# Kernel tuning notes

Hardware: AMD Instinct MI355X
Metric: run time of the kernel (lower is better)

## Reference

```python
import jax, jax.numpy as jnp
import numpy as np

B, T, D, H, V = 256, 32, 500, 1024, 8000
NF = 512  # conv output channels per window size


def setup_inputs() -> dict:
    key = jax.random.key(0)
    ks = jax.random.split(key, 20)
    s = 0.02
    inp = {
        "text": jax.random.normal(ks[0], (B, T, D), jnp.float32),
        "text_bow": jax.random.uniform(ks[1], (B, V), jnp.float32),
        "text_lengths": jax.random.randint(ks[2], (B,), 1, T + 1).astype(jnp.int32),
        # GRU forward direction (PyTorch layout: [3H, D], [3H, H], gates r,z,n)
        "Wih_f": jax.random.normal(ks[3], (3 * H, D), jnp.float32) * s,
        "Whh_f": jax.random.normal(ks[4], (3 * H, H), jnp.float32) * s,
        "bih_f": jax.random.normal(ks[5], (3 * H,), jnp.float32) * s,
        "bhh_f": jax.random.normal(ks[6], (3 * H,), jnp.float32) * s,
        # GRU backward direction
        "Wih_b": jax.random.normal(ks[7], (3 * H, D), jnp.float32) * s,
        "Whh_b": jax.random.normal(ks[8], (3 * H, H), jnp.float32) * s,
        "bih_b": jax.random.normal(ks[9], (3 * H,), jnp.float32) * s,
        "bhh_b": jax.random.normal(ks[10], (3 * H,), jnp.float32) * s,
        # reduce linear: 2H -> H
        "W_red": jax.random.normal(ks[11], (H, 2 * H), jnp.float32) * s,
        "b_red": jax.random.normal(ks[12], (H,), jnp.float32) * s,
        # conv kernels, reshaped from Conv2d [512,1,ws,2H] to 1D conv [512, 2H, ws]
        "conv_w2": jax.random.normal(ks[13], (NF, 2 * H, 2), jnp.float32) * s,
        "conv_b2": jax.random.normal(ks[14], (NF,), jnp.float32) * s,
        "conv_w3": jax.random.normal(ks[15], (NF, 2 * H, 3), jnp.float32) * s,
        "conv_b3": jax.random.normal(ks[16], (NF,), jnp.float32) * s,
        "conv_w4": jax.random.normal(ks[17], (NF, 2 * H, 4), jnp.float32) * s,
        "conv_b4": jax.random.normal(ks[18], (NF,), jnp.float32) * s,
    }
    return inp


def _run_gru_dir(x, lengths, Wih, Whh, bih, bhh, reverse):
    """One GRU direction over padded [B,T,D] with packed-sequence semantics:
    outputs are zero at t >= length (as pad_packed_sequence produces)."""
    b, t, _ = x.shape
    h_dim = Whh.shape[1]
    xg = jnp.einsum('btd,gd->btg', x, Wih) + bih  # [B,T,3H] input projections
    valid = jnp.arange(t)[None, :] < lengths[:, None]  # [B,T]

    def step(h, inp):
        xg_t, v = inp  # [B,3H], [B]
        hg = h @ Whh.T + bhh
        xr, xz, xn = jnp.split(xg_t, 3, axis=-1)
        hr, hz, hn = jnp.split(hg, 3, axis=-1)
        r = jax.nn.sigmoid(xr + hr)
        z = jax.nn.sigmoid(xz + hz)
        n = jnp.tanh(xn + r * hn)
        h_new = (1.0 - z) * n + z * h
        h_new = jnp.where(v[:, None], h_new, h)
        out = jnp.where(v[:, None], h_new, 0.0)
        return h_new, out

    h0 = jnp.zeros((b, h_dim), x.dtype)
    xs = (jnp.swapaxes(xg, 0, 1), valid.T)  # time-major
    _, outs = jax.lax.scan(step, h0, xs, reverse=reverse)
    return jnp.swapaxes(outs, 0, 1)  # [B,T,H]


def _conv_branch(x_c, w, b, ws):
    # x_c: [B, 2H, T]; w: [512, 2H, ws]; 'same-padding-both-sides' (ws-1) like Conv2d padding=(ws-1,0)
    y = jax.lax.conv_general_dilated(
        x_c, w, window_strides=(1,), padding=[(ws - 1, ws - 1)],
        dimension_numbers=('NCH', 'OIH', 'NCH')) + b[None, :, None]
    y = jax.nn.leaky_relu(y, 0.01)
    return jnp.max(y, axis=-1)  # global max-pool over time -> [B,512]


def reference(text, text_bow, text_lengths, Wih_f, Whh_f, bih_f, bhh_f,
              Wih_b, Whh_b, bih_b, bhh_b, W_red, b_red,
              conv_w2, conv_b2, conv_w3, conv_b3, conv_w4, conv_b4):
    out_f = _run_gru_dir(text, text_lengths, Wih_f, Whh_f, bih_f, bhh_f, reverse=False)
    out_b = _run_gru_dir(text, text_lengths, Wih_b, Whh_b, bih_b, bhh_b, reverse=True)
    gru_init_out = jnp.concatenate([out_f, out_b], axis=-1)  # [B,T,2H]

    # masked mean pooling over valid timesteps (the per-sample Python loop)
    mask = (jnp.arange(gru_init_out.shape[1])[None, :] < text_lengths[:, None]).astype(gru_init_out.dtype)
    gru_mean = jnp.sum(gru_init_out * mask[:, :, None], axis=1) / text_lengths[:, None].astype(gru_init_out.dtype)
    gru_out = gru_mean @ W_red.T + b_red  # [B,H] (dropout is identity at eval)

    x_c = jnp.swapaxes(gru_init_out, 1, 2)  # [B,2H,T]
    con_out = jnp.concatenate([
        _conv_branch(x_c, conv_w2, conv_b2, 2),
        _conv_branch(x_c, conv_w3, conv_b3, 3),
        _conv_branch(x_c, conv_w4, conv_b4, 4),
    ], axis=1)  # [B,1536]

    return jnp.concatenate([gru_out, con_out, text_bow], axis=1)  # [B, H+1536+V]
```

## Files before the change

### kernel.cpp

```cpp
#include <hip/hip_runtime.h>
#include <hip/hip_bf16.h>
#include <math.h>

#define B_ 256
#define T_ 32
#define D_ 500
#define H_ 1024
#define V_ 8000
#define NF_ 512
#define G3H (3*H_)
#define H2 (2*H_)
#define OUTC (H_ + 3*NF_ + V_)
#define KPAD 512
#define NTAP 9
#define NCAT (NTAP*NF_)
#define MS 512
#define WFRAG_G (64*32*512)

typedef float f32x4 __attribute__((ext_vector_type(4)));
typedef short bf16x8 __attribute__((ext_vector_type(8)));

static __device__ __forceinline__ short f2b(float f) {
    unsigned u = __float_as_uint(f);
    unsigned r = (u + 0x7fffu + ((u >> 16) & 1u)) >> 16;
    return (short)r;
}
static __device__ __forceinline__ float b2f(short s) {
    return __uint_as_float(((unsigned)(unsigned short)s) << 16);
}

__global__ __launch_bounds__(256) void gemm_bt(
    const short* __restrict__ A, int lda,
    const short* __restrict__ Bt, int ldb,
    const float* __restrict__ bias,
    void* __restrict__ Cv, int ldc,
    int K, int mode)
{
    __shared__ short As[128 * 32];
    __shared__ short Bs[128 * 32];
    const int tid  = threadIdx.x;
    const int w    = tid >> 6, lane = tid & 63;

    const int nbx = gridDim.x;
    const int nwg = nbx * gridDim.y;
    int flat = blockIdx.y * nbx + blockIdx.x;
    flat = (flat & 7) * (nwg >> 3) + (flat >> 3);
    const int m0 = (flat / nbx) * 128, n0 = (flat % nbx) * 128;

    const int wm   = (w >> 1) * 64, wn = (w & 1) * 64;

    f32x4 acc[4][4];
#pragma unroll
    for (int i = 0; i < 4; ++i)
#pragma unroll
        for (int j = 0; j < 4; ++j) acc[i][j] = (f32x4){0.f, 0.f, 0.f, 0.f};

    const int srow = w * 16 + (lane >> 2);
    const int scol = (lane & 3) * 8;
    const long aoff0 = (long)(m0 + srow) * lda + scol;
    const long aoff1 = (long)(m0 + srow + 64) * lda + scol;
    const long boff0 = (long)(n0 + srow) * ldb + scol;
    const long boff1 = (long)(n0 + srow + 64) * ldb + scol;
    short* lA0 = As + w * 512;        short* lA1 = As + 2048 + w * 512;
    short* lB0 = Bs + w * 512;        short* lB1 = Bs + 2048 + w * 512;

    const int fr = lane & 15, fk = (lane >> 4) * 8;

    for (int kt = 0; kt < K; kt += 32) {
        __builtin_amdgcn_global_load_lds((const __attribute__((address_space(1))) void*)(A + aoff0 + kt),
                                         (__attribute__((address_space(3))) void*)lA0, 16, 0, 0);
        __builtin_amdgcn_global_load_lds((const __attribute__((address_space(1))) void*)(A + aoff1 + kt),
                                         (__attribute__((address_space(3))) void*)lA1, 16, 0, 0);
        __builtin_amdgcn_global_load_lds((const __attribute__((address_space(1))) void*)(Bt + boff0 + kt),
                                         (__attribute__((address_space(3))) void*)lB0, 16, 0, 0);
        __builtin_amdgcn_global_load_lds((const __attribute__((address_space(1))) void*)(Bt + boff1 + kt),
                                         (__attribute__((address_space(3))) void*)lB1, 16, 0, 0);
        __syncthreads();
        bf16x8 af[4], bfv[4];
#pragma unroll
        for (int i = 0; i < 4; ++i) af[i]  = *(const bf16x8*)(As + (wm + i * 16 + fr) * 32 + fk);
#pragma unroll
        for (int j = 0; j < 4; ++j) bfv[j] = *(const bf16x8*)(Bs + (wn + j * 16 + fr) * 32 + fk);
#pragma unroll
        for (int i = 0; i < 4; ++i)
#pragma unroll
            for (int j = 0; j < 4; ++j)
                acc[i][j] = __builtin_amdgcn_mfma_f32_16x16x32_bf16(af[i], bfv[j], acc[i][j], 0, 0, 0);
        __syncthreads();
    }

    const int er = (lane >> 4) * 4;
    const int ec = lane & 15;
#pragma unroll
    for (int i = 0; i < 4; ++i) {
#pragma unroll
        for (int j = 0; j < 4; ++j) {
#pragma unroll
            for (int q = 0; q < 4; ++q) {
                const int m = m0 + wm + i * 16 + er + q;
                const int n = n0 + wn + j * 16 + ec;
                float v = acc[i][j][q];
                if (mode == 0) {
                    ((float*)Cv)[(long)m * ldc + n] = v + bias[n];
                } else if (mode == 2) {
                    ((short*)Cv)[(long)m * ldc + n] = f2b(v + bias[n]);
                } else {
                    ((_Float16*)Cv)[(long)m * ldc + n] = (_Float16)v;
                }
            }
        }
    }
}

__global__ void repack_whh(const float* __restrict__ src, short* __restrict__ dst)
{
    const int idx = blockIdx.x * 256 + threadIdx.x;
    const int l = idx & 63;
    const int kt = (idx >> 6) & 31;
    const int j16 = (idx >> 11) & 63;
    const int g = idx >> 17;
    const long srow = ((long)(g << 10) + (j16 << 4) + (l & 15)) * H_ + kt * 32 + ((l >> 4) << 3);
    short o[8];
#pragma unroll
    for (int e = 0; e < 8; ++e) o[e] = f2b(src[srow + e]);
    *(bf16x8*)&dst[(long)idx * 8] = *(bf16x8*)o;
}

__global__ __launch_bounds__(256) void gru_step_frag(
    const short* __restrict__ hbf_prev, short* __restrict__ hbf_next,
    const float* __restrict__ h32_prev, float* __restrict__ h32_next,
    const short* __restrict__ wfragf, const short* __restrict__ wfragb,
    const float* __restrict__ bhhf, const float* __restrict__ bhhb,
    const short* __restrict__ xgf, const short* __restrict__ xgb,
    short* __restrict__ gout, const int* __restrict__ lengths, int s)
{
    const int tid = threadIdx.x;
    const int w = tid >> 6, lane = tid & 63;
    const int bid = blockIdx.x;
    const int jt = bid & 31;
    const int mtd = bid >> 5;
    const int dir = mtd >> 2, mt = mtd & 3;
    const int m0 = dir * 256 + mt * 64;
    const int j0 = jt * 32;
    const int wm = (w >> 1) * 32, wj = (w & 1) * 16;
    const int tt = dir ? (T_ - 1 - s) : s;

    const short* wfrag = dir ? wfragb : wfragf;
    const float* bhh = dir ? bhhb : bhhf;
    const short* xg  = dir ? xgb : xgf;

    const int fr15 = lane & 15, fk8 = (lane >> 4) * 8;
    const long arow0 = (long)(m0 + wm + fr15) * H_ + fk8;
    const long arow1 = arow0 + (long)16 * H_;
    const int j16 = (j0 + wj) >> 4;
    const short* bbase = wfrag + ((long)j16 * 32) * 512 + lane * 8;

    f32x4 acc[3][2];
#pragma unroll
    for (int g = 0; g < 3; ++g)
#pragma unroll
        for (int i = 0; i < 2; ++i) acc[g][i] = (f32x4){0.f, 0.f, 0.f, 0.f};

#pragma unroll 4
    for (int kt = 0; kt < 32; ++kt) {
        const bf16x8 af0 = *(const bf16x8*)(hbf_prev + arow0 + kt * 32);
        const bf16x8 af1 = *(const bf16x8*)(hbf_prev + arow1 + kt * 32);
        const bf16x8 b0 = *(const bf16x8*)(bbase + (long)kt * 512);
        const bf16x8 b1 = *(const bf16x8*)(bbase + (long)kt * 512 + WFRAG_G);
        const bf16x8 b2 = *(const bf16x8*)(bbase + (long)kt * 512 + 2 * WFRAG_G);
        acc[0][0] = __builtin_amdgcn_mfma_f32_16x16x32_bf16(af0, b0, acc[0][0], 0, 0, 0);
        acc[0][1] = __builtin_amdgcn_mfma_f32_16x16x32_bf16(af1, b0, acc[0][1], 0, 0, 0);
        acc[1][0] = __builtin_amdgcn_mfma_f32_16x16x32_bf16(af0, b1, acc[1][0], 0, 0, 0);
        acc[1][1] = __builtin_amdgcn_mfma_f32_16x16x32_bf16(af1, b1, acc[1][1], 0, 0, 0);
        acc[2][0] = __builtin_amdgcn_mfma_f32_16x16x32_bf16(af0, b2, acc[2][0], 0, 0, 0);
        acc[2][1] = __builtin_amdgcn_mfma_f32_16x16x32_bf16(af1, b2, acc[2][1], 0, 0, 0);
    }

    const int er = (lane >> 4) * 4, ec = lane & 15;
    const int jj = j0 + wj + ec;
    const float bhr = bhh[jj], bhz = bhh[H_ + jj], bhn = bhh[2 * H_ + jj];

#pragma unroll
    for (int i = 0; i < 2; ++i) {
#pragma unroll
        for (int q = 0; q < 4; ++q) {
            const int m = m0 + wm + i * 16 + er + q;
            const int b = m & 255;
            const short* xrow = xg + ((long)b * T_ + tt) * G3H;
            const float xr = b2f(xrow[jj]);
            const float xz = b2f(xrow[H_ + jj]);
            const float xn = b2f(xrow[2 * H_ + jj]);
            const float rr = 1.f / (1.f + expf(-(xr + acc[0][i][q] + bhr)));
            const float zz = 1.f / (1.f + expf(-(xz + acc[1][i][q] + bhz)));
            const float nn = tanhf(xn + rr * (acc[2][i][q] + bhn));
            const long hidx = (long)m * H_ + jj;
            const float hp = h32_prev[hidx];
            const float hnew = (1.f - zz) * nn + zz * hp;
            const bool valid = tt < lengths[b];
            const float ho = valid ? hnew : hp;
            h32_next[hidx] = ho;
            hbf_next[hidx] = f2b(ho);
            gout[((long)b * T_ + tt) * H2 + (long)dir * H_ + jj] = valid ? f2b(hnew) : (short)0;
        }
    }
}

__global__ void f2b_pad(const float* __restrict__ src, short* __restrict__ dst,
                        int Ksrc, int Kdst)
{
    const int idx = blockIdx.x * 256 + threadIdx.x;
    const int r = idx / Kdst, c = idx % Kdst;
    dst[idx] = (c < Ksrc) ? f2b(src[(long)r * Ksrc + c]) : (short)0;
}

__global__ void repack_tap(const float* __restrict__ src, short* __restrict__ dst, int ws)
{
    const int idx = blockIdx.x * 256 + threadIdx.x;
    const int rem = idx % (NF_ * H2);
    const int k = idx / (NF_ * H2);
    const int f = rem >> 11, c = rem & 2047;
    dst[idx] = f2b(src[((long)(f << 11) + c) * ws + k]);
}

__global__ void mean_pool2(const short* __restrict__ gin,
                           const int* __restrict__ lengths,
                           short* __restrict__ mean_bf)
{
    const int idx = blockIdx.x * 256 + threadIdx.x;
    const int b = idx >> 11, c = idx & 2047;
    float s = 0.f;
#pragma unroll
    for (int t = 0; t < T_; ++t) s += b2f(gin[((long)(b * T_ + t)) * H2 + c]);
    mean_bf[idx] = f2b(s / (float)lengths[b]);
}

__global__ void conv_max(const _Float16* __restrict__ P,
                         const float* __restrict__ cb2, const float* __restrict__ cb3,
                         const float* __restrict__ cb4, float* __restrict__ out)
{
    const int idx = blockIdx.x * 256 + threadIdx.x;
    const int b = idx / 1536, u0 = idx % 1536;
    int Tout, ws, base, f; float bias;
    if (u0 < 512)       { ws = 2; Tout = 33; base = 0;    f = u0;        bias = cb2[f]; }
    else if (u0 < 1024) { ws = 3; Tout = 34; base = 1024; f = u0 - 512;  bias = cb3[f]; }
    else                { ws = 4; Tout = 35; base = 2560; f = u0 - 1024; bias = cb4[f]; }
    const _Float16* Pb = P + (long)b * T_ * NCAT + base + f;
    float m = -INFINITY;
    for (int u = 0; u < Tout; ++u) {
        float s = bias;
        for (int k = 0; k < ws; ++k) {
            const int t = u - (ws - 1) + k;
            if (t >= 0 && t < T_) s += (float)Pb[(long)t * NCAT + k * NF_];
        }
        s = s > 0.f ? s : 0.01f * s;
        m = fmaxf(m, s);
    }
    out[(long)b * OUTC + H_ + u0] = m;
}

__global__ void bow_copy(const float* __restrict__ bow, float* __restrict__ out)
{
    const int idx = blockIdx.x * 256 + threadIdx.x;
    const int b = idx / 2000, q = idx % 2000;
    const float4* src = (const float4*)(bow + (long)b * V_);
    float4* dst = (float4*)(out + (long)b * OUTC + H_ + 3 * NF_);
    dst[q] = src[q];
}

extern "C" void kernel_launch(void* const* d_in, const int* in_sizes, int n_in,
                              void* d_out, int out_size, void* d_ws, size_t ws_size,
                              hipStream_t stream)
{
    const float* text    = (const float*)d_in[0];
    const float* bow     = (const float*)d_in[1];
    const int*   lengths = (const int*)  d_in[2];
    const float* Wih_f   = (const float*)d_in[3];
    const float* Whh_f   = (const float*)d_in[4];
    const float* bih_f   = (const float*)d_in[5];
    const float* bhh_f   = (const float*)d_in[6];
    const float* Wih_b   = (const float*)d_in[7];
    const float* Whh_b   = (const float*)d_in[8];
    const float* bih_b   = (const float*)d_in[9];
    const float* bhh_b   = (const float*)d_in[10];
    const float* W_red   = (const float*)d_in[11];
    const float* b_red   = (const float*)d_in[12];
    const float* cw2     = (const float*)d_in[13];
    const float* cb2     = (const float*)d_in[14];
    const float* cw3     = (const float*)d_in[15];
    const float* cb3     = (const float*)d_in[16];
    const float* cw4     = (const float*)d_in[17];
    const float* cb4     = (const float*)d_in[18];
    float* out = (float*)d_out;

    char* ws = (char*)d_ws;
    size_t off = 0;
    short* xg_f = (short*)(ws + off); off += (size_t)B_ * T_ * G3H * 2;
    short* xg_b = (short*)(ws + off); off += (size_t)B_ * T_ * G3H * 2;
    _Float16* P    = (_Float16*)(char*)xg_f;
    short* wtap_bf = (short*)((char*)xg_f + (size_t)B_ * T_ * NCAT * 2);
    short* gin_bf = (short*)(ws + off); off += (size_t)B_ * T_ * H2 * 2;
    short* text_bf = gin_bf;
    short* wihf_bf = (short*)((char*)gin_bf + (size_t)B_ * T_ * KPAD * 2);
    short* wihb_bf = wihf_bf + (size_t)G3H * KPAD;
    short* wfragf  = (short*)(ws + off); off += (size_t)3 * WFRAG_G * 2;
    short* wfragb  = (short*)(ws + off); off += (size_t)3 * WFRAG_G * 2;
    short* wred_bf = (short*)(ws + off); off += (size_t)H_ * H2 * 2;
    float* h32     = (float*)(ws + off); off += (size_t)2 * MS * H_ * 4;
    short* h_bf    = (short*)(ws + off); off += (size_t)2 * MS * H_ * 2;
    short* gmean_bf= (short*)(ws + off); off += (size_t)B_ * H2 * 2;

    const dim3 blk(256);

    f2b_pad<<<dim3((B_ * T_ * KPAD) / 256), blk, 0, stream>>>(text, text_bf, D_, KPAD);
    f2b_pad<<<dim3((G3H * KPAD) / 256), blk, 0, stream>>>(Wih_f, wihf_bf, D_, KPAD);
    f2b_pad<<<dim3((G3H * KPAD) / 256), blk, 0, stream>>>(Wih_b, wihb_bf, D_, KPAD);
    f2b_pad<<<dim3((H_ * H2) / 256), blk, 0, stream>>>(W_red, wred_bf, H2, H2);
    repack_whh<<<dim3(1536), blk, 0, stream>>>(Whh_f, wfragf);
    repack_whh<<<dim3(1536), blk, 0, stream>>>(Whh_b, wfragb);

    gemm_bt<<<dim3(G3H / 128, (B_ * T_) / 128), blk, 0, stream>>>(
        text_bf, KPAD, wihf_bf, KPAD, bih_f, xg_f, G3H, KPAD, 2);
    gemm_bt<<<dim3(G3H / 128, (B_ * T_) / 128), blk, 0, stream>>>(
        text_bf, KPAD, wihb_bf, KPAD, bih_b, xg_b, G3H, KPAD, 2);

    hipMemsetAsync(h32, 0, (size_t)MS * H_ * 4, stream);
    hipMemsetAsync(h_bf, 0, (size_t)MS * H_ * 2, stream);
    for (int s = 0; s < T_; ++s) {
        const int cur = s & 1, nxt = (s + 1) & 1;
        gru_step_frag<<<dim3(256), blk, 0, stream>>>(
            h_bf + (size_t)cur * MS * H_, h_bf + (size_t)nxt * MS * H_,
            h32 + (size_t)cur * MS * H_, h32 + (size_t)nxt * MS * H_,
            wfragf, wfragb, bhh_f, bhh_b, xg_f, xg_b,
            gin_bf, lengths, s);
    }

    mean_pool2<<<dim3((B_ * H2) / 256), blk, 0, stream>>>(gin_bf, lengths, gmean_bf);
    gemm_bt<<<dim3(H_ / 128, B_ / 128), blk, 0, stream>>>(
        gmean_bf, H2, wred_bf, H2, b_red, out, OUTC, H2, 0);

    repack_tap<<<dim3((2 * NF_ * H2) / 256), blk, 0, stream>>>(cw2, wtap_bf, 2);
    repack_tap<<<dim3((3 * NF_ * H2) / 256), blk, 0, stream>>>(cw3, wtap_bf + (size_t)2 * NF_ * H2, 3);
    repack_tap<<<dim3((4 * NF_ * H2) / 256), blk, 0, stream>>>(cw4, wtap_bf + (size_t)5 * NF_ * H2, 4);
    gemm_bt<<<dim3(NCAT / 128, (B_ * T_) / 128), blk, 0, stream>>>(
        gin_bf, H2, wtap_bf, H2, nullptr, P, NCAT, H2, 3);

    conv_max<<<dim3((B_ * 1536) / 256), blk, 0, stream>>>(P, cb2, cb3, cb4, out);
    bow_copy<<<dim3((B_ * 2000) / 256), blk, 0, stream>>>(bow, out);
}
```

Before: 1.076 ms.

## Merge fwd/bwd input GEMMs and halve GRU step M-tile for more blocks

```diff
diff --git a/kernel.cpp b/kernel.cpp
--- a/kernel.cpp
+++ b/kernel.cpp
@@ -9,6 +9,7 @@
 #define V_ 8000
 #define NF_ 512
 #define G3H (3*H_)
+#define G6H (6*H_)
 #define H2 (2*H_)
 #define OUTC (H_ + 3*NF_ + V_)
 #define KPAD 512
@@ -131,49 +132,41 @@
     const float* __restrict__ h32_prev, float* __restrict__ h32_next,
     const short* __restrict__ wfragf, const short* __restrict__ wfragb,
     const float* __restrict__ bhhf, const float* __restrict__ bhhb,
-    const short* __restrict__ xgf, const short* __restrict__ xgb,
+    const short* __restrict__ xgcat,
     short* __restrict__ gout, const int* __restrict__ lengths, int s)
 {
     const int tid = threadIdx.x;
     const int w = tid >> 6, lane = tid & 63;
     const int bid = blockIdx.x;
     const int jt = bid & 31;
-    const int mtd = bid >> 5;
-    const int dir = mtd >> 2, mt = mtd & 3;
-    const int m0 = dir * 256 + mt * 64;
+    const int mq = bid >> 5;
+    const int dir = mq >> 3, mt = mq & 7;
+    const int m0 = dir * 256 + mt * 32;
     const int j0 = jt * 32;
-    const int wm = (w >> 1) * 32, wj = (w & 1) * 16;
+    const int wm = (w >> 1) * 16, wj = (w & 1) * 16;
     const int tt = dir ? (T_ - 1 - s) : s;
 
     const short* wfrag = dir ? wfragb : wfragf;
     const float* bhh = dir ? bhhb : bhhf;
-    const short* xg  = dir ? xgb : xgf;
 
     const int fr15 = lane & 15, fk8 = (lane >> 4) * 8;
-    const long arow0 = (long)(m0 + wm + fr15) * H_ + fk8;
-    const long arow1 = arow0 + (long)16 * H_;
+    const long arow = (long)(m0 + wm + fr15) * H_ + fk8;
     const int j16 = (j0 + wj) >> 4;
     const short* bbase = wfrag + ((long)j16 * 32) * 512 + lane * 8;
 
-    f32x4 acc[3][2];
-#pragma unroll
-    for (int g = 0; g < 3; ++g)
-#pragma unroll
-        for (int i = 0; i < 2; ++i) acc[g][i] = (f32x4){0.f, 0.f, 0.f, 0.f};
-
-#pragma unroll 4
+    f32x4 acc[3];
+#pragma unroll
+    for (int g = 0; g < 3; ++g) acc[g] = (f32x4){0.f, 0.f, 0.f, 0.f};
+
+#pragma unroll 8
     for (int kt = 0; kt < 32; ++kt) {
-        const bf16x8 af0 = *(const bf16x8*)(hbf_prev + arow0 + kt * 32);
-        const bf16x8 af1 = *(const bf16x8*)(hbf_prev + arow1 + kt * 32);
+        const bf16x8 af0 = *(const bf16x8*)(hbf_prev + arow + kt * 32);
         const bf16x8 b0 = *(const bf16x8*)(bbase + (long)kt * 512);
         const bf16x8 b1 = *(const bf16x8*)(bbase + (long)kt * 512 + WFRAG_G);
         const bf16x8 b2 = *(const bf16x8*)(bbase + (long)kt * 512 + 2 * WFRAG_G);
-        acc[0][0] = __builtin_amdgcn_mfma_f32_16x16x32_bf16(af0, b0, acc[0][0], 0, 0, 0);
-        acc[0][1] = __builtin_amdgcn_mfma_f32_16x16x32_bf16(af1, b0, acc[0][1], 0, 0, 0);
-        acc[1][0] = __builtin_amdgcn_mfma_f32_16x16x32_bf16(af0, b1, acc[1][0], 0, 0, 0);
-        acc[1][1] = __builtin_amdgcn_mfma_f32_16x16x32_bf16(af1, b1, acc[1][1], 0, 0, 0);
-        acc[2][0] = __builtin_amdgcn_mfma_f32_16x16x32_bf16(af0, b2, acc[2][0], 0, 0, 0);
-        acc[2][1] = __builtin_amdgcn_mfma_f32_16x16x32_bf16(af1, b2, acc[2][1], 0, 0, 0);
+        acc[0] = __builtin_amdgcn_mfma_f32_16x16x32_bf16(af0, b0, acc[0], 0, 0, 0);
+        acc[1] = __builtin_amdgcn_mfma_f32_16x16x32_bf16(af0, b1, acc[1], 0, 0, 0);
+        acc[2] = __builtin_amdgcn_mfma_f32_16x16x32_bf16(af0, b2, acc[2], 0, 0, 0);
     }
 
     const int er = (lane >> 4) * 4, ec = lane & 15;
@@ -181,27 +174,24 @@
     const float bhr = bhh[jj], bhz = bhh[H_ + jj], bhn = bhh[2 * H_ + jj];
 
 #pragma unroll
-    for (int i = 0; i < 2; ++i) {
-#pragma unroll
-        for (int q = 0; q < 4; ++q) {
-            const int m = m0 + wm + i * 16 + er + q;
-            const int b = m & 255;
-            const short* xrow = xg + ((long)b * T_ + tt) * G3H;
-            const float xr = b2f(xrow[jj]);
-            const float xz = b2f(xrow[H_ + jj]);
-            const float xn = b2f(xrow[2 * H_ + jj]);
-            const float rr = 1.f / (1.f + expf(-(xr + acc[0][i][q] + bhr)));
-            const float zz = 1.f / (1.f + expf(-(xz + acc[1][i][q] + bhz)));
-            const float nn = tanhf(xn + rr * (acc[2][i][q] + bhn));
-            const long hidx = (long)m * H_ + jj;
-            const float hp = h32_prev[hidx];
-            const float hnew = (1.f - zz) * nn + zz * hp;
-            const bool valid = tt < lengths[b];
-            const float ho = valid ? hnew : hp;
-            h32_next[hidx] = ho;
-            hbf_next[hidx] = f2b(ho);
-            gout[((long)b * T_ + tt) * H2 + (long)dir * H_ + jj] = valid ? f2b(hnew) : (short)0;
-        }
+    for (int q = 0; q < 4; ++q) {
+        const int m = m0 + wm + er + q;
+        const int b = m & 255;
+        const short* xrow = xgcat + ((long)b * T_ + tt) * G6H + (long)dir * G3H;
+        const float xr = b2f(xrow[jj]);
+        const float xz = b2f(xrow[H_ + jj]);
+        const float xn = b2f(xrow[2 * H_ + jj]);
+        const float rr = 1.f / (1.f + expf(-(xr + acc[0][q] + bhr)));
+        const float zz = 1.f / (1.f + expf(-(xz + acc[1][q] + bhz)));
+        const float nn = tanhf(xn + rr * (acc[2][q] + bhn));
+        const long hidx = (long)m * H_ + jj;
+        const float hp = h32_prev[hidx];
+        const float hnew = (1.f - zz) * nn + zz * hp;
+        const bool valid = tt < lengths[b];
+        const float ho = valid ? hnew : hp;
+        h32_next[hidx] = ho;
+        hbf_next[hidx] = f2b(ho);
+        gout[((long)b * T_ + tt) * H2 + (long)dir * H_ + jj] = valid ? f2b(hnew) : (short)0;
     }
 }
 
@@ -211,6 +201,13 @@
     const int idx = blockIdx.x * 256 + threadIdx.x;
     const int r = idx / Kdst, c = idx % Kdst;
     dst[idx] = (c < Ksrc) ? f2b(src[(long)r * Ksrc + c]) : (short)0;
+}
+
+__global__ void cat_bias(const float* __restrict__ a, const float* __restrict__ b,
+                         float* __restrict__ dst)
+{
+    const int idx = blockIdx.x * 256 + threadIdx.x;
+    dst[idx] = (idx < G3H) ? a[idx] : b[idx - G3H];
 }
 
 __global__ void repack_tap(const float* __restrict__ src, short* __restrict__ dst, int ws)
@@ -294,10 +291,9 @@
 
     char* ws = (char*)d_ws;
     size_t off = 0;
-    short* xg_f = (short*)(ws + off); off += (size_t)B_ * T_ * G3H * 2;
-    short* xg_b = (short*)(ws + off); off += (size_t)B_ * T_ * G3H * 2;
-    _Float16* P    = (_Float16*)(char*)xg_f;
-    short* wtap_bf = (short*)((char*)xg_f + (size_t)B_ * T_ * NCAT * 2);
+    short* xgcat = (short*)(ws + off); off += (size_t)B_ * T_ * G6H * 2;
+    _Float16* P    = (_Float16*)(char*)xgcat;
+    short* wtap_bf = (short*)((char*)xgcat + (size_t)B_ * T_ * NCAT * 2);
     short* gin_bf = (short*)(ws + off); off += (size_t)B_ * T_ * H2 * 2;
     short* text_bf = gin_bf;
     short* wihf_bf = (short*)((char*)gin_bf + (size_t)B_ * T_ * KPAD * 2);
@@ -308,6 +304,7 @@
     float* h32     = (float*)(ws + off); off += (size_t)2 * MS * H_ * 4;
     short* h_bf    = (short*)(ws + off); off += (size_t)2 * MS * H_ * 2;
     short* gmean_bf= (short*)(ws + off); off += (size_t)B_ * H2 * 2;
+    float* bih_cat = (float*)(ws + off); off += (size_t)G6H * 4;
 
     const dim3 blk(256);
 
@@ -315,22 +312,21 @@
     f2b_pad<<<dim3((G3H * KPAD) / 256), blk, 0, stream>>>(Wih_f, wihf_bf, D_, KPAD);
     f2b_pad<<<dim3((G3H * KPAD) / 256), blk, 0, stream>>>(Wih_b, wihb_bf, D_, KPAD);
     f2b_pad<<<dim3((H_ * H2) / 256), blk, 0, stream>>>(W_red, wred_bf, H2, H2);
+    cat_bias<<<dim3(G6H / 256), blk, 0, stream>>>(bih_f, bih_b, bih_cat);
     repack_whh<<<dim3(1536), blk, 0, stream>>>(Whh_f, wfragf);
     repack_whh<<<dim3(1536), blk, 0, stream>>>(Whh_b, wfragb);
 
-    gemm_bt<<<dim3(G3H / 128, (B_ * T_) / 128), blk, 0, stream>>>(
-        text_bf, KPAD, wihf_bf, KPAD, bih_f, xg_f, G3H, KPAD, 2);
-    gemm_bt<<<dim3(G3H / 128, (B_ * T_) / 128), blk, 0, stream>>>(
-        text_bf, KPAD, wihb_bf, KPAD, bih_b, xg_b, G3H, KPAD, 2);
+    gemm_bt<<<dim3(G6H / 128, (B_ * T_) / 128), blk, 0, stream>>>(
+        text_bf, KPAD, wihf_bf, KPAD, bih_cat, xgcat, G6H, KPAD, 2);
 
     hipMemsetAsync(h32, 0, (size_t)MS * H_ * 4, stream);
     hipMemsetAsync(h_bf, 0, (size_t)MS * H_ * 2, stream);
     for (int s = 0; s < T_; ++s) {
         const int cur = s & 1, nxt = (s + 1) & 1;
-        gru_step_frag<<<dim3(256), blk, 0, stream>>>(
+        gru_step_frag<<<dim3(512), blk, 0, stream>>>(
             h_bf + (size_t)cur * MS * H_, h_bf + (size_t)nxt * MS * H_,
             h32 + (size_t)cur * MS * H_, h32 + (size_t)nxt * MS * H_,
-            wfragf, wfragb, bhh_f, bhh_b, xg_f, xg_b,
+            wfragf, wfragb, bhh_f, bhh_b, xgcat,
             gin_bf, lengths, s);
     }
 
```

Result: slower. 1.193 ms (+10.9%).

## Merge forward/backward input projections into one GEMM and prefetch GRU epilogue operands

Applied to the files above, without the earlier changes.

```diff
diff --git a/kernel.cpp b/kernel.cpp
--- a/kernel.cpp
+++ b/kernel.cpp
@@ -9,6 +9,7 @@
 #define V_ 8000
 #define NF_ 512
 #define G3H (3*H_)
+#define G6H (6*H_)
 #define H2 (2*H_)
 #define OUTC (H_ + 3*NF_ + V_)
 #define KPAD 512
@@ -105,7 +106,7 @@
                 } else if (mode == 2) {
                     ((short*)Cv)[(long)m * ldc + n] = f2b(v + bias[n]);
                 } else {
-                    ((_Float16*)Cv)[(long)m * ldc + n] = (_Float16)v;
+                    __builtin_nontemporal_store((_Float16)v, (_Float16*)Cv + (long)m * ldc + n);
                 }
             }
         }
@@ -131,7 +132,7 @@
     const float* __restrict__ h32_prev, float* __restrict__ h32_next,
     const short* __restrict__ wfragf, const short* __restrict__ wfragb,
     const float* __restrict__ bhhf, const float* __restrict__ bhhb,
-    const short* __restrict__ xgf, const short* __restrict__ xgb,
+    const short* __restrict__ xgcat,
     short* __restrict__ gout, const int* __restrict__ lengths, int s)
 {
     const int tid = threadIdx.x;
@@ -147,13 +148,33 @@
 
     const short* wfrag = dir ? wfragb : wfragf;
     const float* bhh = dir ? bhhb : bhhf;
-    const short* xg  = dir ? xgb : xgf;
 
     const int fr15 = lane & 15, fk8 = (lane >> 4) * 8;
     const long arow0 = (long)(m0 + wm + fr15) * H_ + fk8;
     const long arow1 = arow0 + (long)16 * H_;
     const int j16 = (j0 + wj) >> 4;
     const short* bbase = wfrag + ((long)j16 * 32) * 512 + lane * 8;
+
+    const int er = (lane >> 4) * 4, ec = lane & 15;
+    const int jj = j0 + wj + ec;
+
+    float xr[2][4], xz[2][4], xn[2][4], hp[2][4];
+    int lenv[2][4];
+#pragma unroll
+    for (int i = 0; i < 2; ++i) {
+#pragma unroll
+        for (int q = 0; q < 4; ++q) {
+            const int m = m0 + wm + i * 16 + er + q;
+            const int b = m & 255;
+            const short* xrow = xgcat + ((long)b * T_ + tt) * G6H + (long)dir * G3H;
+            xr[i][q] = b2f(xrow[jj]);
+            xz[i][q] = b2f(xrow[H_ + jj]);
+            xn[i][q] = b2f(xrow[2 * H_ + jj]);
+            hp[i][q] = h32_prev[(long)m * H_ + jj];
+            lenv[i][q] = lengths[b];
+        }
+    }
+    const float bhr = bhh[jj], bhz = bhh[H_ + jj], bhn = bhh[2 * H_ + jj];
 
     f32x4 acc[3][2];
 #pragma unroll
@@ -176,28 +197,19 @@
         acc[2][1] = __builtin_amdgcn_mfma_f32_16x16x32_bf16(af1, b2, acc[2][1], 0, 0, 0);
     }
 
-    const int er = (lane >> 4) * 4, ec = lane & 15;
-    const int jj = j0 + wj + ec;
-    const float bhr = bhh[jj], bhz = bhh[H_ + jj], bhn = bhh[2 * H_ + jj];
-
 #pragma unroll
     for (int i = 0; i < 2; ++i) {
 #pragma unroll
         for (int q = 0; q < 4; ++q) {
             const int m = m0 + wm + i * 16 + er + q;
             const int b = m & 255;
-            const short* xrow = xg + ((long)b * T_ + tt) * G3H;
-            const float xr = b2f(xrow[jj]);
-            const float xz = b2f(xrow[H_ + jj]);
-            const float xn = b2f(xrow[2 * H_ + jj]);
-            const float rr = 1.f / (1.f + expf(-(xr + acc[0][i][q] + bhr)));
-            const float zz = 1.f / (1.f + expf(-(xz + acc[1][i][q] + bhz)));
-            const float nn = tanhf(xn + rr * (acc[2][i][q] + bhn));
+            const float rr = 1.f / (1.f + expf(-(xr[i][q] + acc[0][i][q] + bhr)));
+            const float zz = 1.f / (1.f + expf(-(xz[i][q] + acc[1][i][q] + bhz)));
+            const float nn = tanhf(xn[i][q] + rr * (acc[2][i][q] + bhn));
+            const float hnew = (1.f - zz) * nn + zz * hp[i][q];
+            const bool valid = tt < lenv[i][q];
+            const float ho = valid ? hnew : hp[i][q];
             const long hidx = (long)m * H_ + jj;
-            const float hp = h32_prev[hidx];
-            const float hnew = (1.f - zz) * nn + zz * hp;
-            const bool valid = tt < lengths[b];
-            const float ho = valid ? hnew : hp;
             h32_next[hidx] = ho;
             hbf_next[hidx] = f2b(ho);
             gout[((long)b * T_ + tt) * H2 + (long)dir * H_ + jj] = valid ? f2b(hnew) : (short)0;
@@ -211,6 +223,13 @@
     const int idx = blockIdx.x * 256 + threadIdx.x;
     const int r = idx / Kdst, c = idx % Kdst;
     dst[idx] = (c < Ksrc) ? f2b(src[(long)r * Ksrc + c]) : (short)0;
+}
+
+__global__ void cat_bias(const float* __restrict__ a, const float* __restrict__ b,
+                         float* __restrict__ dst)
+{
+    const int idx = blockIdx.x * 256 + threadIdx.x;
+    dst[idx] = (idx < G3H) ? a[idx] : b[idx - G3H];
 }
 
 __global__ void repack_tap(const float* __restrict__ src, short* __restrict__ dst, int ws)
@@ -294,10 +313,9 @@
 
     char* ws = (char*)d_ws;
     size_t off = 0;
-    short* xg_f = (short*)(ws + off); off += (size_t)B_ * T_ * G3H * 2;
-    short* xg_b = (short*)(ws + off); off += (size_t)B_ * T_ * G3H * 2;
-    _Float16* P    = (_Float16*)(char*)xg_f;
-    short* wtap_bf = (short*)((char*)xg_f + (size_t)B_ * T_ * NCAT * 2);
+    short* xgcat = (short*)(ws + off); off += (size_t)B_ * T_ * G6H * 2;
+    _Float16* P    = (_Float16*)(char*)xgcat;
+    short* wtap_bf = (short*)((char*)xgcat + (size_t)B_ * T_ * NCAT * 2);
     short* gin_bf = (short*)(ws + off); off += (size_t)B_ * T_ * H2 * 2;
     short* text_bf = gin_bf;
     short* wihf_bf = (short*)((char*)gin_bf + (size_t)B_ * T_ * KPAD * 2);
@@ -308,6 +326,7 @@
     float* h32     = (float*)(ws + off); off += (size_t)2 * MS * H_ * 4;
     short* h_bf    = (short*)(ws + off); off += (size_t)2 * MS * H_ * 2;
     short* gmean_bf= (short*)(ws + off); off += (size_t)B_ * H2 * 2;
+    float* bih_cat = (float*)(ws + off); off += (size_t)G6H * 4;
 
     const dim3 blk(256);
 
@@ -315,13 +334,12 @@
     f2b_pad<<<dim3((G3H * KPAD) / 256), blk, 0, stream>>>(Wih_f, wihf_bf, D_, KPAD);
     f2b_pad<<<dim3((G3H * KPAD) / 256), blk, 0, stream>>>(Wih_b, wihb_bf, D_, KPAD);
     f2b_pad<<<dim3((H_ * H2) / 256), blk, 0, stream>>>(W_red, wred_bf, H2, H2);
+    cat_bias<<<dim3(G6H / 256), blk, 0, stream>>>(bih_f, bih_b, bih_cat);
     repack_whh<<<dim3(1536), blk, 0, stream>>>(Whh_f, wfragf);
     repack_whh<<<dim3(1536), blk, 0, stream>>>(Whh_b, wfragb);
 
-    gemm_bt<<<dim3(G3H / 128, (B_ * T_) / 128), blk, 0, stream>>>(
-        text_bf, KPAD, wihf_bf, KPAD, bih_f, xg_f, G3H, KPAD, 2);
-    gemm_bt<<<dim3(G3H / 128, (B_ * T_) / 128), blk, 0, stream>>>(
-        text_bf, KPAD, wihb_bf, KPAD, bih_b, xg_b, G3H, KPAD, 2);
+    gemm_bt<<<dim3(G6H / 128, (B_ * T_) / 128), blk, 0, stream>>>(
+        text_bf, KPAD, wihf_bf, KPAD, bih_cat, xgcat, G6H, KPAD, 2);
 
     hipMemsetAsync(h32, 0, (size_t)MS * H_ * 4, stream);
     hipMemsetAsync(h_bf, 0, (size_t)MS * H_ * 2, stream);
@@ -330,7 +348,7 @@
         gru_step_frag<<<dim3(256), blk, 0, stream>>>(
             h_bf + (size_t)cur * MS * H_, h_bf + (size_t)nxt * MS * H_,
             h32 + (size_t)cur * MS * H_, h32 + (size_t)nxt * MS * H_,
-            wfragf, wfragb, bhh_f, bhh_b, xg_f, xg_b,
+            wfragf, wfragb, bhh_f, bhh_b, xgcat,
             gin_bf, lengths, s);
     }
 
```

New measurement: 1.274 ms. 18.4% more time.

## Add 256x256-tile GEMM with 4-stage direct-to-LDS pipeline for input and conv GEMMs

Applied to the files above, without the earlier changes.

```diff
diff --git a/kernel.cpp b/kernel.cpp
--- a/kernel.cpp
+++ b/kernel.cpp
@@ -27,6 +27,116 @@
 }
 static __device__ __forceinline__ float b2f(short s) {
     return __uint_as_float(((unsigned)(unsigned short)s) << 16);
+}
+
+template<int MODE>
+__global__ __launch_bounds__(512) void gemm256(
+    const short* __restrict__ A, int lda,
+    const short* __restrict__ Bt, int ldb,
+    const float* __restrict__ bias,
+    void* __restrict__ Cv, int ldc, int K)
+{
+    __shared__ short As[4][256 * 32];
+    __shared__ short Bs[4][256 * 32];
+    const int tid = threadIdx.x;
+    const int w = tid >> 6, lane = tid & 63;
+
+    const int nbx = gridDim.x;
+    const int nwg = nbx * gridDim.y;
+    int flat = blockIdx.y * nbx + blockIdx.x;
+    flat = (flat & 7) * (nwg >> 3) + (flat >> 3);
+    const int m0 = (flat / nbx) * 256, n0 = (flat % nbx) * 256;
+
+    const int wm = (w >> 2) * 128;
+    const int wn = (w & 3) * 64;
+
+    const int srow = w * 16 + (lane >> 2);
+    const int scol = (lane & 3) * 8;
+    const long aoff = (long)(m0 + srow) * lda + scol;
+    const long boff = (long)(n0 + srow) * ldb + scol;
+
+#define STAGE256(t_, buf_) do { \
+    const long ka_ = (long)(t_) * 32; \
+    __builtin_amdgcn_global_load_lds((const __attribute__((address_space(1))) void*)(A + aoff + ka_), \
+        (__attribute__((address_space(3))) void*)(&As[buf_][w * 512]), 16, 0, 0); \
+    __builtin_amdgcn_global_load_lds((const __attribute__((address_space(1))) void*)(A + aoff + (long)128 * lda + ka_), \
+        (__attribute__((address_space(3))) void*)(&As[buf_][4096 + w * 512]), 16, 0, 0); \
+    __builtin_amdgcn_global_load_lds((const __attribute__((address_space(1))) void*)(Bt + boff + ka_), \
+        (__attribute__((address_space(3))) void*)(&Bs[buf_][w * 512]), 16, 0, 0); \
+    __builtin_amdgcn_global_load_lds((const __attribute__((address_space(1))) void*)(Bt + boff + (long)128 * ldb + ka_), \
+        (__attribute__((address_space(3))) void*)(&Bs[buf_][4096 + w * 512]), 16, 0, 0); \
+} while (0)
+
+    f32x4 acc[8][4];
+#pragma unroll
+    for (int i = 0; i < 8; ++i)
+#pragma unroll
+        for (int j = 0; j < 4; ++j) acc[i][j] = (f32x4){0.f, 0.f, 0.f, 0.f};
+
+    const int fr = lane & 15, fk = (lane >> 4) * 8;
+    const int T = K >> 5;
+
+    STAGE256(0, 0);
+    STAGE256(1, 1);
+    STAGE256(2, 2);
+    asm volatile("s_waitcnt vmcnt(8)" ::: "memory");
+    asm volatile("s_barrier" ::: "memory");
+
+    for (int t = 0; t < T; ++t) {
+        const int buf = t & 3;
+        if (t + 3 < T) STAGE256(t + 3, (t + 3) & 3);
+
+        bf16x8 af[4], bfv[4];
+#pragma unroll
+        for (int i = 0; i < 4; ++i)
+            af[i] = *(const bf16x8*)(&As[buf][(wm + i * 16 + fr) * 32 + fk]);
+#pragma unroll
+        for (int j = 0; j < 4; ++j)
+            bfv[j] = *(const bf16x8*)(&Bs[buf][(wn + j * 16 + fr) * 32 + fk]);
+        __builtin_amdgcn_s_setprio(1);
+#pragma unroll
+        for (int i = 0; i < 4; ++i)
+#pragma unroll
+            for (int j = 0; j < 4; ++j)
+                acc[i][j] = __builtin_amdgcn_mfma_f32_16x16x32_bf16(af[i], bfv[j], acc[i][j], 0, 0, 0);
+        __builtin_amdgcn_s_setprio(0);
+        asm volatile("s_barrier" ::: "memory");
+
+#pragma unroll
+        for (int i = 0; i < 4; ++i)
+            af[i] = *(const bf16x8*)(&As[buf][(wm + 64 + i * 16 + fr) * 32 + fk]);
+        __builtin_amdgcn_s_setprio(1);
+#pragma unroll
+        for (int i = 0; i < 4; ++i)
+#pragma unroll
+            for (int j = 0; j < 4; ++j)
+                acc[4 + i][j] = __builtin_amdgcn_mfma_f32_16x16x32_bf16(af[i], bfv[j], acc[4 + i][j], 0, 0, 0);
+        __builtin_amdgcn_s_setprio(0);
+
+        if (t < T - 3)      asm volatile("s_waitcnt vmcnt(8)" ::: "memory");
+        else if (t == T - 3) asm volatile("s_waitcnt vmcnt(4)" ::: "memory");
+        else if (t == T - 2) asm volatile("s_waitcnt vmcnt(0)" ::: "memory");
+        asm volatile("s_barrier" ::: "memory");
+    }
+#undef STAGE256
+
+    const int er = (lane >> 4) * 4, ec = lane & 15;
+#pragma unroll
+    for (int i = 0; i < 8; ++i) {
+#pragma unroll
+        for (int j = 0; j < 4; ++j) {
+#pragma unroll
+            for (int q = 0; q < 4; ++q) {
+                const int m = m0 + wm + i * 16 + er + q;
+                const int n = n0 + wn + j * 16 + ec;
+                const float v = acc[i][j][q];
+                if (MODE == 2)
+                    ((short*)Cv)[(long)m * ldc + n] = f2b(v + bias[n]);
+                else
+                    ((_Float16*)Cv)[(long)m * ldc + n] = (_Float16)v;
+            }
+        }
+    }
 }
 
 __global__ __launch_bounds__(256) void gemm_bt(
@@ -318,10 +428,10 @@
     repack_whh<<<dim3(1536), blk, 0, stream>>>(Whh_f, wfragf);
     repack_whh<<<dim3(1536), blk, 0, stream>>>(Whh_b, wfragb);
 
-    gemm_bt<<<dim3(G3H / 128, (B_ * T_) / 128), blk, 0, stream>>>(
-        text_bf, KPAD, wihf_bf, KPAD, bih_f, xg_f, G3H, KPAD, 2);
-    gemm_bt<<<dim3(G3H / 128, (B_ * T_) / 128), blk, 0, stream>>>(
-        text_bf, KPAD, wihb_bf, KPAD, bih_b, xg_b, G3H, KPAD, 2);
+    gemm256<2><<<dim3(G3H / 256, (B_ * T_) / 256), dim3(512), 0, stream>>>(
+        text_bf, KPAD, wihf_bf, KPAD, bih_f, xg_f, G3H, KPAD);
+    gemm256<2><<<dim3(G3H / 256, (B_ * T_) / 256), dim3(512), 0, stream>>>(
+        text_bf, KPAD, wihb_bf, KPAD, bih_b, xg_b, G3H, KPAD);
 
     hipMemsetAsync(h32, 0, (size_t)MS * H_ * 4, stream);
     hipMemsetAsync(h_bf, 0, (size_t)MS * H_ * 2, stream);
@@ -341,8 +451,8 @@
     repack_tap<<<dim3((2 * NF_ * H2) / 256), blk, 0, stream>>>(cw2, wtap_bf, 2);
     repack_tap<<<dim3((3 * NF_ * H2) / 256), blk, 0, stream>>>(cw3, wtap_bf + (size_t)2 * NF_ * H2, 3);
     repack_tap<<<dim3((4 * NF_ * H2) / 256), blk, 0, stream>>>(cw4, wtap_bf + (size_t)5 * NF_ * H2, 4);
-    gemm_bt<<<dim3(NCAT / 128, (B_ * T_) / 128), blk, 0, stream>>>(
-        gin_bf, H2, wtap_bf, H2, nullptr, P, NCAT, H2, 3);
+    gemm256<3><<<dim3(NCAT / 256, (B_ * T_) / 256), dim3(512), 0, stream>>>(
+        gin_bf, H2, wtap_bf, H2, nullptr, P, NCAT, H2);
 
     conv_max<<<dim3((B_ * 1536) / 256), blk, 0, stream>>>(P, cb2, cb3, cb4, out);
     bow_copy<<<dim3((B_ * 2000) / 256), blk, 0, stream>>>(bow, out);
```

New measurement: 1.098 ms. 1.02x slower.
